# Kernel tuning notes

Measured on AMD Instinct MI355X. Metric: run time of the kernel, lower is better.

## Reference

```python
import jax, jax.numpy as jnp
import numpy as np

N, E, S, TS = 12, 7, 1024, 3          # num_boxes, edge_types, state_dim, time_step
D_IN = 1056 * 1 * 5 * 5               # emb_features * continuous_frames * crop_size^2


def _gru(x, h0, Wih, Whh, bih, bhh):
    """PyTorch-order GRU (gates r,z,n) over leading time axis. x: [T, B, S]."""
    def step(h, xt):
        gi = xt @ Wih.T + bih
        gh = h @ Whh.T + bhh
        ir, iz, inn = jnp.split(gi, 3, axis=-1)
        hr, hz, hn = jnp.split(gh, 3, axis=-1)
        r = jax.nn.sigmoid(ir + hr)
        z = jax.nn.sigmoid(iz + hz)
        n = jnp.tanh(inn + r * hn)
        h_new = (1.0 - z) * n + z * h
        return h_new, h_new
    _, ys = jax.lax.scan(step, h0, x)
    return ys


def _forward(pose_features, Wc, bc, We, be, Wcomp, bcomp, Wr, br, Wz, bz, Wh, bh,
             Wih, Whh, bih, bhh, Wa, ba):
    B, T = pose_features.shape[:2]
    BT, BNN = B * T, B * N * N
    # compress_fc: [BT, N, D_IN] -> [BT, N, S]
    prop = pose_features.reshape(BT, N, D_IN) @ Wc.T + bc
    # torch code xavier-normal-inits the GRU h0 each call; we use deterministic keys.
    h0_std = (2.0 / (BNN * S + S)) ** 0.5
    base = jax.random.key(42)
    gs = None
    for t in range(TS + 1):
        # all edge_fcs at once: [BT, N, E, S]
        msgs = jnp.einsum('bnd,esd->bnes', prop, We) + be
        msg_flat = msgs.reshape(BT, N * E, S)       # index n*E+e, matches torch cat+view
        scs = []
        for e in range(E):
            rf = msgs[:, :, e, :]                   # [BT, N, S]
            pair = jnp.concatenate([
                jnp.broadcast_to(rf[:, :, None, :], (BT, N, N, S)),
                jnp.broadcast_to(rf[:, None, :, :], (BT, N, N, S))], axis=-1)
            # -> [T, B*N*N, 2S] (permute(1,0,2,3,4) in torch)
            pair = pair.reshape(B, T, N, N, 2 * S).transpose(1, 0, 2, 3, 4).reshape(T, BNN, 2 * S)
            x = pair @ Wcomp.T + bcomp              # compress: [T, BNN, S]
            h0 = jax.random.normal(jax.random.fold_in(base, t * E + e), (BNN, S), dtype=x.dtype) * h0_std
            y = _gru(x, h0, Wih, Whh, bih, bhh)     # [T, BNN, S]
            y = y.reshape(T, B, N, N, S).transpose(1, 0, 2, 3, 4).reshape(BT, N, N, S)
            # edge attention (Dropout is identity in eval): sigmoid(linear->1)
            scs.append(jax.nn.sigmoid(jnp.einsum('bmns,s->bmn', y, Wa[e]) + ba[e]))
        gs = jnp.stack(scs, axis=-1)                # [BT, N, N, E]
        merged = jnp.einsum('bnm,bms->bns', gs.reshape(BT, N, N * E), msg_flat)
        a = jnp.concatenate([merged, prop], axis=-1)
        r = jax.nn.sigmoid(a @ Wr.T + br)
        z = jax.nn.sigmoid(a @ Wz.T + bz)
        h_hat = jnp.tanh(jnp.concatenate([merged, r * prop], axis=-1) @ Wh.T + bh)
        prop = (1.0 - z) * prop + z * h_hat
    box_states = gs                                 # last graph_scores
    action_score = ((1.0 - box_states[..., :1]) * box_states).sum(axis=2).reshape(B, T, N, E)
    actor_score = (1.0 - box_states[..., 0]).reshape(B, T, N, N)
    acty_score = jax.nn.softmax(
        (action_score * actor_score.sum(axis=-1)[..., None]).sum(axis=2)[:, :, 1:], axis=-1)
    return action_score, acty_score, actor_score


def setup_inputs() -> dict:
    key = jax.random.key(0)
    ks = jax.random.split(key, 16)
    B, T = 2, 4
    k = 1.0 / np.sqrt(S)  # torch GRU default uniform init bound
    return {
        'pose_features': jax.random.normal(ks[0], (B, T, N, D_IN), jnp.float32),
        'boxes_in': jax.random.uniform(ks[1], (B, T, N, 4), jnp.float32),
        'boxes_dhdw': jax.random.normal(ks[2], (B, T, N, 2), jnp.float32),
        'bboxes_num_in': jax.random.randint(ks[3], (B, T), 1, N),
        'actor_label': jax.random.randint(ks[4], (B, T, N), 0, E),
        'Wc': 0.01 * jax.random.normal(ks[5], (S, D_IN), jnp.float32),
        'bc': jnp.zeros((S,), jnp.float32),
        'We': 0.01 * jax.random.normal(ks[6], (E, S, S), jnp.float32),
        'be': jnp.zeros((E, S), jnp.float32),
        'Wcomp': 0.01 * jax.random.normal(ks[7], (S, 2 * S), jnp.float32),
        'bcomp': jnp.zeros((S,), jnp.float32),
        'Wr': 0.01 * jax.random.normal(ks[8], (S, 2 * S), jnp.float32),
        'br': jnp.zeros((S,), jnp.float32),
        'Wz': 0.01 * jax.random.normal(ks[9], (S, 2 * S), jnp.float32),
        'bz': jnp.zeros((S,), jnp.float32),
        'Wh': 0.01 * jax.random.normal(ks[10], (S, 2 * S), jnp.float32),
        'bh': jnp.zeros((S,), jnp.float32),
        'Wih': jax.random.uniform(ks[11], (3 * S, S), jnp.float32, -k, k),
        'Whh': jax.random.uniform(ks[12], (3 * S, S), jnp.float32, -k, k),
        'bih': jax.random.uniform(ks[13], (3 * S,), jnp.float32, -k, k),
        'bhh': jax.random.uniform(ks[14], (3 * S,), jnp.float32, -k, k),
        'Wa': 0.01 * jax.random.normal(ks[15], (E, S), jnp.float32),
        'ba': jnp.zeros((E,), jnp.float32),
    }


def reference(pose_features, boxes_in, boxes_dhdw, bboxes_num_in, actor_label,
              Wc, bc, We, be, Wcomp, bcomp, Wr, br, Wz, bz, Wh, bh,
              Wih, Whh, bih, bhh, Wa, ba):
    # boxes_in / boxes_dhdw / bboxes_num_in / actor_label only provide shapes in eval mode
    del boxes_in, boxes_dhdw, bboxes_num_in, actor_label
    return _forward(pose_features, Wc, bc, We, be, Wcomp, bcomp, Wr, br, Wz, bz,
                    Wh, bh, Wih, Whh, bih, bhh, Wa, ba)
```

## Files before the change

kernel.cpp:

```cpp
#include <hip/hip_runtime.h>
#include <math.h>

#define NQ 12
#define EQ 7
#define SQ 1024
#define TSQ 3
#define DIN 26400
#define BQ 2
#define TQ 4
#define BT 8
#define BNN 288
#define NROWS 2016
#define G3S 3072
#define BK 32

typedef unsigned short u16;
typedef float f32x4 __attribute__((ext_vector_type(4)));
typedef short s16x8 __attribute__((ext_vector_type(8)));

__device__ __forceinline__ short bh(float f) {
    unsigned u = __float_as_uint(f);
    return (short)((u + 0x8000u) >> 16);
}
__device__ __forceinline__ float b2f(u16 u) {
    return __uint_as_float((unsigned)u << 16);
}
__device__ __forceinline__ s16x8 pack8(float4 a, float4 b) {
    s16x8 r;
    r[0] = bh(a.x); r[1] = bh(a.y); r[2] = bh(a.z); r[3] = bh(a.w);
    r[4] = bh(b.x); r[5] = bh(b.y); r[6] = bh(b.z); r[7] = bh(b.w);
    return r;
}
__device__ __forceinline__ void gload16(const void* g, void* l) {
    __builtin_amdgcn_global_load_lds(
        (const __attribute__((address_space(1))) unsigned*)g,
        (__attribute__((address_space(3))) unsigned*)l, 16, 0, 0);
}
__device__ inline float sigmoidf(float x) { return 1.f / (1.f + expf(-x)); }

template<int AS32, int BS32>
__global__ __launch_bounds__(256)
void gemm_mfma(const void* __restrict__ Ap, long sAb, int lda,
               const void* __restrict__ Bp, long sBb, int ldb,
               const float* __restrict__ bias, long sBiasb,
               float* __restrict__ C, long sCb, int ldc,
               u16* __restrict__ Cb, long sCbb, int ldcb,
               int M, int Nn, int K, int act, int ksplit)
{
    __shared__ __align__(16) u16 lA[2][256][8];
    __shared__ __align__(16) u16 lB[2][512][8];

    const int z = blockIdx.z;
    const int az = z / ksplit;
    const int ks = z - az * ksplit;
    const int Ksl = K / ksplit;
    const int kbase = ks * Ksl;

    const char* Abase = (const char*)Ap + (long)az * sAb * (AS32 ? 4 : 2);
    const char* Bbase = (const char*)Bp + (long)az * sBb * (BS32 ? 4 : 2);

    const int tid = threadIdx.x;
    const int lane = tid & 63;
    const int wave = tid >> 6;
    const int row0 = blockIdx.x * 64;
    const int col0 = blockIdx.y * 128;
    const int wcol = wave * 32;

    const int akg = tid >> 6;
    long arow = row0 + (tid & 63); if (arow >= M) arow = M - 1;
    const int bkg0 = tid >> 7;
    const int s1 = tid + 256;
    const int bkg1 = s1 >> 7;
    long brow0 = col0 + (tid & 127); if (brow0 >= Nn) brow0 = Nn - 1;
    long brow1 = col0 + (s1 & 127);  if (brow1 >= Nn) brow1 = Nn - 1;

    const int arw32 = tid >> 2, akg32 = tid & 3;
    long ar32 = row0 + arw32; if (ar32 >= M) ar32 = M - 1;
    const int brw32 = tid >> 1, bh32 = tid & 1;
    long br32 = col0 + brw32; if (br32 >= Nn) br32 = Nn - 1;

    f32x4 acc[4][2] = {};

#define STAGE(b, kt) do {                                                     \
    const int k0_ = kbase + (kt) * BK;                                        \
    if constexpr (AS32) {                                                     \
        const float* A32 = (const float*)Abase;                               \
        const float* p0 = A32 + ar32 * lda + k0_ + akg32 * 8;                 \
        *(s16x8*)&lA[b][akg32 * 64 + arw32][0] =                              \
            pack8(*(const float4*)p0, *(const float4*)(p0 + 4));              \
    } else {                                                                  \
        const u16* A16 = (const u16*)Abase;                                   \
        gload16(A16 + arow * lda + k0_ + akg * 8, &lA[b][tid][0]);            \
    }                                                                         \
    if constexpr (BS32) {                                                     \
        const float* B32 = (const float*)Bbase;                               \
        const float* q0 = B32 + br32 * ldb + k0_ + bh32 * 16;                 \
        *(s16x8*)&lB[b][(bh32 * 2) * 128 + brw32][0] =                        \
            pack8(*(const float4*)q0, *(const float4*)(q0 + 4));              \
        *(s16x8*)&lB[b][(bh32 * 2 + 1) * 128 + brw32][0] =                    \
            pack8(*(const float4*)(q0 + 8), *(const float4*)(q0 + 12));       \
    } else {                                                                  \
        const u16* B16 = (const u16*)Bbase;                                   \
        gload16(B16 + brow0 * ldb + k0_ + bkg0 * 8, &lB[b][tid][0]);          \
        gload16(B16 + brow1 * ldb + k0_ + bkg1 * 8, &lB[b][s1][0]);           \
    }                                                                         \
} while (0)

    const int nk = Ksl / BK;
    STAGE(0, 0);
    __syncthreads();
    int buf = 0;
    const int kg = lane >> 4;
    const int lr = lane & 15;
    for (int kt = 0; kt < nk; ++kt) {
        if (kt + 1 < nk) STAGE(buf ^ 1, kt + 1);
        s16x8 af[4], bfr[2];
#pragma unroll
        for (int m = 0; m < 4; ++m)
            af[m] = *(const s16x8*)&lA[buf][kg * 64 + m * 16 + lr][0];
#pragma unroll
        for (int n = 0; n < 2; ++n)
            bfr[n] = *(const s16x8*)&lB[buf][kg * 128 + wcol + n * 16 + lr][0];
#pragma unroll
        for (int m = 0; m < 4; ++m)
#pragma unroll
            for (int n = 0; n < 2; ++n)
                acc[m][n] = __builtin_amdgcn_mfma_f32_16x16x32_bf16(af[m], bfr[n], acc[m][n], 0, 0, 0);
        __syncthreads();
        buf ^= 1;
    }
#undef STAGE

    const int ccol = lane & 15;
    const int crow = (lane >> 4) * 4;
#pragma unroll
    for (int n = 0; n < 2; ++n) {
        const int c = col0 + wcol + n * 16 + ccol;
        const float bv = bias ? bias[(long)az * sBiasb + c] : 0.f;
#pragma unroll
        for (int m = 0; m < 4; ++m) {
            const int rb = row0 + m * 16 + crow;
#pragma unroll
            for (int q = 0; q < 4; ++q) {
                const int r = rb + q;
                if (r >= M) continue;
                float v = acc[m][n][q] + bv;
                if (act == 1) v = 1.f / (1.f + expf(-v));
                else if (act == 2) v = tanhf(v);
                if (C)  C[(long)z * sCb + (long)r * ldc + c] = v;
                if (Cb) Cb[(long)z * sCbb + (long)r * ldcb + c] = (u16)bh(v);
            }
        }
    }
}

__global__ __launch_bounds__(256)
void gemm128_f32(const float* __restrict__ A, int lda,
                 const float* __restrict__ Bm, int ldb,
                 float* __restrict__ C, long sCb, int ldc,
                 u16* __restrict__ Cb, int ldcb,
                 int M, int Nn, int K, int ksplit)
{
    __shared__ __align__(16) u16 lA[2][512][8];
    __shared__ __align__(16) u16 lB[2][512][8];

    const int ks = blockIdx.z;
    const int Ksl = K / ksplit;
    const int kbase = ks * Ksl;

    const int tid = threadIdx.x;
    const int lane = tid & 63;
    const int wave = tid >> 6;
    const int row0 = blockIdx.x * 128;
    const int col0 = blockIdx.y * 128;
    const int wrow = (wave >> 1) * 64;
    const int wcol = (wave & 1) * 64;

    const int rw = tid >> 1, hf = tid & 1;
    long ar = row0 + rw; if (ar >= M) ar = M - 1;
    long br = col0 + rw; if (br >= Nn) br = Nn - 1;

    f32x4 acc[4][4] = {};

#define STAGE128(b, kt) do {                                                  \
    const int k0_ = kbase + (kt) * BK;                                        \
    const float* p = A + ar * lda + k0_ + hf * 16;                            \
    *(s16x8*)&lA[b][(hf * 2) * 128 + rw][0] =                                 \
        pack8(*(const float4*)p, *(const float4*)(p + 4));                    \
    *(s16x8*)&lA[b][(hf * 2 + 1) * 128 + rw][0] =                             \
        pack8(*(const float4*)(p + 8), *(const float4*)(p + 12));             \
    const float* q = Bm + br * ldb + k0_ + hf * 16;                           \
    *(s16x8*)&lB[b][(hf * 2) * 128 + rw][0] =                                 \
        pack8(*(const float4*)q, *(const float4*)(q + 4));                    \
    *(s16x8*)&lB[b][(hf * 2 + 1) * 128 + rw][0] =                             \
        pack8(*(const float4*)(q + 8), *(const float4*)(q + 12));             \
} while (0)

    const int nk = Ksl / BK;
    STAGE128(0, 0);
    __syncthreads();
    int buf = 0;
    const int kg = lane >> 4;
    const int lr = lane & 15;
    for (int kt = 0; kt < nk; ++kt) {
        if (kt + 1 < nk) STAGE128(buf ^ 1, kt + 1);
        s16x8 af[4], bfr[4];
#pragma unroll
        for (int m = 0; m < 4; ++m)
            af[m] = *(const s16x8*)&lA[buf][kg * 128 + wrow + m * 16 + lr][0];
#pragma unroll
        for (int n = 0; n < 4; ++n)
            bfr[n] = *(const s16x8*)&lB[buf][kg * 128 + wcol + n * 16 + lr][0];
#pragma unroll
        for (int m = 0; m < 4; ++m)
#pragma unroll
            for (int n = 0; n < 4; ++n)
                acc[m][n] = __builtin_amdgcn_mfma_f32_16x16x32_bf16(af[m], bfr[n], acc[m][n], 0, 0, 0);
        __syncthreads();
        buf ^= 1;
    }
#undef STAGE128

    const int ccol = lane & 15;
    const int crow = (lane >> 4) * 4;
#pragma unroll
    for (int n = 0; n < 4; ++n) {
        const int c = col0 + wcol + n * 16 + ccol;
#pragma unroll
        for (int m = 0; m < 4; ++m) {
            const int rb = row0 + wrow + m * 16 + crow;
#pragma unroll
            for (int q = 0; q < 4; ++q) {
                const int r = rb + q;
                if (r >= M) continue;
                float v = acc[m][n][q];
                if (C)  C[(long)ks * sCb + (long)r * ldc + c] = v;
                if (Cb) Cb[(long)r * ldcb + c] = (u16)bh(v);
            }
        }
    }
}

__global__ __launch_bounds__(512)
void gh_gru(const u16* __restrict__ hb_in, const u16* __restrict__ Whh_b,
            const float* __restrict__ bhh, const u16* __restrict__ Gnm_b,
            const float* __restrict__ cbias,
            float* __restrict__ h, u16* __restrict__ hb_out,
            const float* __restrict__ Wa, float* __restrict__ gs_part, int tt)
{
    __shared__ __align__(16) u16 lA[2][1024][8];
    __shared__ __align__(16) u16 lB[2][1536][8];
    __shared__ float rowdot[128];

    const int f = blockIdx.x;
    const int ly = 2 * (f & 7) + ((f >> 3) & 1);
    const int lx = f >> 4;
    const int row0 = lx * 128;
    const int col0 = ly * 64;

    const int tid = threadIdx.x;
    const int lane = tid & 63;
    const int wave = tid >> 6;
    const int wr = wave >> 1;
    const int wc = wave & 1;

    long arow = row0 + (tid & 127); if (arow >= NROWS) arow = NROWS - 1;

    const u16* aP0 = hb_in + arow * SQ + (tid >> 7) * 8;
    const u16* aP1 = aP0 + 32;
    const u16* bP[3];
#pragma unroll
    for (int j = 0; j < 3; ++j) {
        const int s = tid + j * 512;
        const int bk16 = s / 192;
        const int grow = s - bk16 * 192;
        bP[j] = Whh_b + (long)((grow >> 6) * SQ + col0 + (grow & 63)) * SQ + bk16 * 8;
    }

    f32x4 acc[3][2][2] = {};

#define GSTAGE(b, kt) do {                                                    \
    const int k0_ = (kt) * 64;                                                \
    gload16(aP0 + k0_, &lA[b][tid][0]);                                       \
    gload16(aP1 + k0_, &lA[b][tid + 512][0]);                                 \
    _Pragma("unroll")                                                         \
    for (int j = 0; j < 3; ++j)                                               \
        gload16(bP[j] + k0_, &lB[b][tid + j * 512][0]);                       \
} while (0)

    GSTAGE(0, 0);
    __syncthreads();
    int buf = 0;
    const int kg = lane >> 4;
    const int lr = lane & 15;
    for (int kt = 0; kt < 16; ++kt) {
        if (kt + 1 < 16) GSTAGE(buf ^ 1, kt + 1);
#pragma unroll
        for (int kk = 0; kk < 2; ++kk) {
            const int k16 = kk * 4 + kg;
            s16x8 af[2], bfr[3][2];
#pragma unroll
            for (int m = 0; m < 2; ++m)
                af[m] = *(const s16x8*)&lA[buf][k16 * 128 + wr * 32 + m * 16 + lr][0];
#pragma unroll
            for (int g = 0; g < 3; ++g)
#pragma unroll
                for (int n = 0; n < 2; ++n)
                    bfr[g][n] = *(const s16x8*)&lB[buf][k16 * 192 + g * 64 + wc * 32 + n * 16 + lr][0];
#pragma unroll
            for (int g = 0; g < 3; ++g)
#pragma unroll
                for (int m = 0; m < 2; ++m)
#pragma unroll
                    for (int n = 0; n < 2; ++n)
                        acc[g][m][n] = __builtin_amdgcn_mfma_f32_16x16x32_bf16(af[m], bfr[g][n], acc[g][m][n], 0, 0, 0);
        }
        __syncthreads();
        buf ^= 1;
    }
#undef GSTAGE

    if (tid < 128) rowdot[tid] = 0.f;
    __syncthreads();

    const int ccol = lane & 15;
    const int crow4 = (lane >> 4) * 4;
    int col2[2];
    float cbv[3][2], bhv[3][2];
#pragma unroll
    for (int n = 0; n < 2; ++n) {
        const int c = col0 + wc * 32 + n * 16 + ccol;
        col2[n] = c;
#pragma unroll
        for (int g = 0; g < 3; ++g) {
            cbv[g][n] = cbias[g * SQ + c];
            bhv[g][n] = bhh[g * SQ + c];
        }
    }

#pragma unroll
    for (int m = 0; m < 2; ++m) {
#pragma unroll
        for (int q = 0; q < 4; ++q) {
            const int row = row0 + wr * 32 + m * 16 + crow4 + q;
            const bool valid = (row < NROWS);
            float d = 0.f;
            if (valid) {
                const int e = row / BNN;
                const int rr = row - e * BNN;
                const int b_ = rr / 144;
                const int ni = (rr / 12) % 12;
                const int mi = rr % 12;
                const int bt = b_ * TQ + tt;
                const u16* gnp = Gnm_b + ((long)e * 96 + bt * 12 + ni) * 6144;
                const u16* gmp = Gnm_b + ((long)e * 96 + bt * 12 + mi) * 6144 + G3S;
                const float* wap = Wa + (long)e * SQ;
#pragma unroll
                for (int n = 0; n < 2; ++n) {
                    const int c = col2[n];
                    float gr  = acc[0][m][n][q] + bhv[0][n] + b2f(gnp[c]) + b2f(gmp[c]) + cbv[0][n];
                    float gz  = acc[1][m][n][q] + bhv[1][n] + b2f(gnp[SQ + c]) + b2f(gmp[SQ + c]) + cbv[1][n];
                    float ghn = acc[2][m][n][q] + bhv[2][n];
                    float gin = b2f(gnp[2 * SQ + c]) + b2f(gmp[2 * SQ + c]) + cbv[2][n];
                    float rg = sigmoidf(gr);
                    float zg = sigmoidf(gz);
                    float nn2 = tanhf(gin + rg * ghn);
                    float hp = h[(long)row * SQ + c];
                    float hn = (1.f - zg) * nn2 + zg * hp;
                    h[(long)row * SQ + c] = hn;
                    hb_out[(long)row * SQ + c] = (u16)bh(hn);
                    d += hn * wap[c];
                }
            }
            d += __shfl_xor(d, 1); d += __shfl_xor(d, 2);
            d += __shfl_xor(d, 4); d += __shfl_xor(d, 8);
            if (valid && ccol == 0)
                atomicAdd(&rowdot[wr * 32 + m * 16 + crow4 + q], d);
        }
    }
    __syncthreads();
    if (tid < 128) {
        const int row = row0 + tid;
        if (row < NROWS) gs_part[((long)tt * 2048 + row) * 16 + ly] = rowdot[tid];
    }
}

__global__ __launch_bounds__(256)
void gru0(const u16* __restrict__ Gnm_b, const float* __restrict__ cbias,
          const float* __restrict__ bhh,
          float* __restrict__ h, u16* __restrict__ hb_out,
          const float* __restrict__ Wa, const float* __restrict__ ba,
          float* __restrict__ gs)
{
    const int row = blockIdx.x;
    const int e = row / BNN;
    const int r = row % BNN;
    const int b_ = r / 144;
    const int ni = (r / 12) % 12;
    const int mi = r % 12;
    const int bt = b_ * TQ;

    const u16* gnp = Gnm_b + ((long)e * 96 + bt * 12 + ni) * 6144;
    const u16* gmp = Gnm_b + ((long)e * 96 + bt * 12 + mi) * 6144 + G3S;
    float* hp = h + (long)row * SQ;
    u16* hpb = hb_out + (long)row * SQ;

    const int s = threadIdx.x * 4;

    ushort4 nR = *(const ushort4*)(gnp + s);
    ushort4 nZ = *(const ushort4*)(gnp + SQ + s);
    ushort4 nN = *(const ushort4*)(gnp + 2 * SQ + s);
    ushort4 mR = *(const ushort4*)(gmp + s);
    ushort4 mZ = *(const ushort4*)(gmp + SQ + s);
    ushort4 mN = *(const ushort4*)(gmp + 2 * SQ + s);
    float4 cbR = *(const float4*)(cbias + s);
    float4 cbZ = *(const float4*)(cbias + SQ + s);
    float4 cbN = *(const float4*)(cbias + 2 * SQ + s);
    float4 bhR = *(const float4*)(bhh + s);
    float4 bhZ = *(const float4*)(bhh + SQ + s);
    float4 bhN = *(const float4*)(bhh + 2 * SQ + s);
    float4 wv  = *(const float4*)(Wa + (long)e * SQ + s);

    float4 hn4;
    float dot = 0.f;

#define GRU0_COMP(c, u)                                                       \
    {                                                                         \
        float rg = sigmoidf(b2f(nR.u) + b2f(mR.u) + cbR.c + bhR.c);           \
        float zg = sigmoidf(b2f(nZ.u) + b2f(mZ.u) + cbZ.c + bhZ.c);           \
        float nn = tanhf(b2f(nN.u) + b2f(mN.u) + cbN.c + rg * bhN.c);         \
        float hn = (1.f - zg) * nn;                                           \
        hn4.c = hn;                                                           \
        dot += hn * wv.c;                                                     \
    }
    GRU0_COMP(x, x) GRU0_COMP(y, y) GRU0_COMP(z, z) GRU0_COMP(w, w)
#undef GRU0_COMP

    *(float4*)(hp + s) = hn4;
    ushort4 hb4;
    hb4.x = (u16)bh(hn4.x); hb4.y = (u16)bh(hn4.y);
    hb4.z = (u16)bh(hn4.z); hb4.w = (u16)bh(hn4.w);
    *(ushort4*)(hpb + s) = hb4;

    for (int off = 32; off > 0; off >>= 1) dot += __shfl_down(dot, off);
    __shared__ float red[4];
    if ((threadIdx.x & 63) == 0) red[threadIdx.x >> 6] = dot;
    __syncthreads();
    if (threadIdx.x == 0) {
        float tot = red[0] + red[1] + red[2] + red[3] + ba[e];
        gs[((bt * 12 + ni) * 12 + mi) * EQ + e] = sigmoidf(tot);
    }
}

__global__ void gs_fin_all(const float* __restrict__ gs_part, const float* __restrict__ ba,
                           float* __restrict__ gs)
{
    int idx = blockIdx.x * 256 + threadIdx.x;
    if (idx >= 3 * 2048) return;
    const int tt = 1 + (idx >> 11);
    const int row = idx & 2047;
    if (row >= NROWS) return;
    float s = 0.f;
#pragma unroll
    for (int j = 0; j < 16; ++j) s += gs_part[((long)tt * 2048 + row) * 16 + j];
    const int e = row / BNN;
    const int rr = row - e * BNN;
    const int b_ = rr / 144;
    const int ni = (rr / 12) % 12;
    const int mi = rr % 12;
    const int bt = b_ * TQ + tt;
    gs[((bt * 12 + ni) * 12 + mi) * EQ + e] = sigmoidf(s + ba[e]);
}

__global__ __launch_bounds__(256)
void reduce_k(const float* __restrict__ part, int ksplit, int mn, int Nn,
              const float* __restrict__ bias, long sBiasB, int act,
              float* __restrict__ Cf, long sCfB, int ldcf,
              u16* __restrict__ Cb, long sCbB, int ldcb)
{
    int i4 = blockIdx.x * 256 + threadIdx.x;
    int total4 = mn >> 2;
    if (i4 >= total4) return;
    int b = blockIdx.y;
    const float4* p4 = (const float4*)part;
    float4 s = make_float4(0.f, 0.f, 0.f, 0.f);
    for (int ks = 0; ks < ksplit; ++ks) {
        float4 v = p4[(long)(b * ksplit + ks) * total4 + i4];
        s.x += v.x; s.y += v.y; s.z += v.z; s.w += v.w;
    }
    int i = i4 << 2;
    int r = i / Nn, c = i % Nn;
    if (bias) {
        float4 bv = *(const float4*)(bias + (long)b * sBiasB + c);
        s.x += bv.x; s.y += bv.y; s.z += bv.z; s.w += bv.w;
    }
    if (act == 1) {
        s.x = sigmoidf(s.x); s.y = sigmoidf(s.y); s.z = sigmoidf(s.z); s.w = sigmoidf(s.w);
    } else if (act == 2) {
        s.x = tanhf(s.x); s.y = tanhf(s.y); s.z = tanhf(s.z); s.w = tanhf(s.w);
    }
    if (Cf) *(float4*)(Cf + (long)b * sCfB + (long)r * ldcf + c) = s;
    if (Cb) {
        ushort4 o;
        o.x = (u16)bh(s.x); o.y = (u16)bh(s.y); o.z = (u16)bh(s.z); o.w = (u16)bh(s.w);
        *(ushort4*)(Cb + (long)b * sCbB + (long)r * ldcb + c) = o;
    }
}

__global__ void cvt_bf16_k(const float* __restrict__ src, u16* __restrict__ dst, int n4)
{
    int i = blockIdx.x * 256 + threadIdx.x;
    if (i >= n4) return;
    float4 v = ((const float4*)src)[i];
    ushort4 o;
    o.x = (u16)bh(v.x); o.y = (u16)bh(v.y); o.z = (u16)bh(v.z); o.w = (u16)bh(v.w);
    ((ushort4*)dst)[i] = o;
}

__global__ __launch_bounds__(256)
void transpose_wc(const float* __restrict__ Wcomp, float* __restrict__ W1T, float* __restrict__ W2T)
{
    __shared__ float t1[32][33];
    __shared__ float t2[32][33];
    const int tx = threadIdx.x & 31;
    const int ty = threadIdx.x >> 5;
    const int d0 = blockIdx.x * 32;
    const int s0 = blockIdx.y * 32;
#pragma unroll
    for (int k = 0; k < 4; ++k) {
        int d = d0 + ty + k * 8;
        t1[ty + k * 8][tx] = Wcomp[(long)d * 2048 + s0 + tx];
        t2[ty + k * 8][tx] = Wcomp[(long)d * 2048 + 1024 + s0 + tx];
    }
    __syncthreads();
#pragma unroll
    for (int k = 0; k < 4; ++k) {
        int s = s0 + ty + k * 8;
        W1T[(long)s * 1024 + d0 + tx] = t1[tx][ty + k * 8];
        W2T[(long)s * 1024 + d0 + tx] = t2[tx][ty + k * 8];
    }
}

__global__ void pack_rz(const float* __restrict__ Wr, const float* __restrict__ Wz,
                        const float* __restrict__ br, const float* __restrict__ bz,
                        u16* __restrict__ Wrz, float* __restrict__ brz)
{
    int i4 = blockIdx.x * 256 + threadIdx.x;
    if (i4 < 512) {
        int c = i4 * 4;
        float4 b = (c < 1024) ? *(const float4*)(br + c) : *(const float4*)(bz + c - 1024);
        *(float4*)(brz + c) = b;
    }
    if (i4 >= 1048576) return;
    int i = i4 * 4;
    int j = i >> 11;
    int c = i & 2047;
    float4 v = (j < 1024) ? *(const float4*)(Wr + (long)j * 2048 + c)
                          : *(const float4*)(Wz + (long)(j - 1024) * 2048 + c);
    ushort4 o;
    o.x = (u16)bh(v.x); o.y = (u16)bh(v.y); o.z = (u16)bh(v.z); o.w = (u16)bh(v.w);
    *(ushort4*)(Wrz + i) = o;
}

__global__ void cbias_k(const float* __restrict__ Wih, const float* __restrict__ bih,
                        const float* __restrict__ bcomp, float* __restrict__ cbias)
{
    int g = blockIdx.x * blockDim.x + threadIdx.x;
    if (g >= G3S) return;
    const float* w = Wih + (long)g * SQ;
    float s = 0.f;
    for (int k = 0; k < SQ; k += 4) {
        float4 wv = *(const float4*)(w + k);
        float4 bv = *(const float4*)(bcomp + k);
        s += wv.x * bv.x + wv.y * bv.y + wv.z * bv.z + wv.w * bv.w;
    }
    cbias[g] = s + bih[g];
}

__global__ __launch_bounds__(256)
void merged_amat_k(const float* __restrict__ gs, const u16* __restrict__ msgs_b,
                   const float* __restrict__ prop, u16* __restrict__ amat_b)
{
    const int bn = blockIdx.x;
    const int bt = bn / 12;
    __shared__ float g[84];
    if (threadIdx.x < 84) g[threadIdx.x] = gs[bn * 84 + threadIdx.x];
    __syncthreads();
    const int s = threadIdx.x * 4;
    float4 acc = make_float4(0.f, 0.f, 0.f, 0.f);
    for (int j = 0; j < 84; ++j) {
        const ushort4 mv = *(const ushort4*)(msgs_b + ((long)(bt * 84 + j)) * SQ + s);
        float gj = g[j];
        acc.x += gj * b2f(mv.x);
        acc.y += gj * b2f(mv.y);
        acc.z += gj * b2f(mv.z);
        acc.w += gj * b2f(mv.w);
    }
    ushort4 o;
    o.x = (u16)bh(acc.x); o.y = (u16)bh(acc.y); o.z = (u16)bh(acc.z); o.w = (u16)bh(acc.w);
    *(ushort4*)(amat_b + (long)bn * 2048 + s) = o;
    float4 pv = *(const float4*)(prop + (long)bn * SQ + s);
    ushort4 o2;
    o2.x = (u16)bh(pv.x); o2.y = (u16)bh(pv.y); o2.z = (u16)bh(pv.z); o2.w = (u16)bh(pv.w);
    *(ushort4*)(amat_b + (long)bn * 2048 + 1024 + s) = o2;
}

__global__ void ahat_k(const float* __restrict__ rz, const float* __restrict__ prop,
                       u16* __restrict__ amat_b)
{
    int i = blockIdx.x * 256 + threadIdx.x;
    int rrow = i >> 10, c = i & 1023;
    float r = rz[(long)rrow * 2048 + c];
    amat_b[(long)rrow * 2048 + 1024 + c] = (u16)bh(r * prop[i]);
}

__global__ void propupd_k(const float* __restrict__ rz, const float* __restrict__ hhat,
                          float* __restrict__ prop, u16* __restrict__ prop_b)
{
    int i = blockIdx.x * 256 + threadIdx.x;
    int rrow = i >> 10, c = i & 1023;
    float z = rz[(long)rrow * 2048 + 1024 + c];
    float v = (1.f - z) * prop[i] + z * hhat[i];
    prop[i] = v;
    prop_b[i] = (u16)bh(v);
}

__global__ __launch_bounds__(256)
void outputs_k(const float* __restrict__ gs, float* __restrict__ out)
{
    __shared__ float s_act[672];
    __shared__ float s_asum[96];
    int tid = threadIdx.x;
    for (int idx = tid; idx < 672; idx += 256) {
        int bn = idx / 7, e = idx % 7;
        float sum = 0.f;
        for (int m = 0; m < 12; ++m) {
            float g0 = gs[bn * 84 + m * 7];
            sum += (1.f - g0) * gs[bn * 84 + m * 7 + e];
        }
        s_act[idx] = sum;
        out[idx] = sum;
    }
    for (int idx = tid; idx < 96; idx += 256) {
        float a = 0.f;
        for (int m = 0; m < 12; ++m) a += 1.f - gs[idx * 84 + m * 7];
        s_asum[idx] = a;
    }
    for (int idx = tid; idx < 1152; idx += 256) {
        int bn = idx / 12, m = idx % 12;
        out[720 + idx] = 1.f - gs[bn * 84 + m * 7];
    }
    __syncthreads();
    if (tid < 8) {
        float tmp[6];
        float mx = -1e30f;
        for (int e = 1; e < 7; ++e) {
            float sum = 0.f;
            for (int n = 0; n < 12; ++n) {
                int bn = tid * 12 + n;
                sum += s_act[bn * 7 + e] * s_asum[bn];
            }
            tmp[e - 1] = sum;
            mx = fmaxf(mx, sum);
        }
        float den = 0.f;
        for (int e = 0; e < 6; ++e) { tmp[e] = expf(tmp[e] - mx); den += tmp[e]; }
        for (int e = 0; e < 6; ++e) out[672 + tid * 6 + e] = tmp[e] / den;
    }
}

template<int AS32, int BS32>
static void launch_gemm(const void* A, long sAb, int lda,
                        const void* B, long sBb, int ldb,
                        const float* bias, long sBiasb,
                        float* C, long sCb, int ldc,
                        u16* Cb, long sCbb, int ldcb,
                        int M, int Nn, int K, int act, int batch, int ksplit,
                        hipStream_t stream)
{
    dim3 grid((M + 63) / 64, (Nn + 127) / 128, batch * ksplit);
    gemm_mfma<AS32, BS32><<<grid, dim3(256), 0, stream>>>(
        A, sAb, lda, B, sBb, ldb, bias, sBiasb, C, sCb, ldc, Cb, sCbb, ldcb,
        M, Nn, K, act, ksplit);
}

extern "C" void kernel_launch(void* const* d_in, const int* in_sizes, int n_in,
                              void* d_out, int out_size, void* d_ws, size_t ws_size,
                              hipStream_t stream)
{
    const float* pose  = (const float*)d_in[0];
    const float* Wc    = (const float*)d_in[5];
    const float* bc    = (const float*)d_in[6];
    const float* We    = (const float*)d_in[7];
    const float* be    = (const float*)d_in[8];
    const float* Wcomp = (const float*)d_in[9];
    const float* bcomp = (const float*)d_in[10];
    const float* Wr    = (const float*)d_in[11];
    const float* br    = (const float*)d_in[12];
    const float* Wz    = (const float*)d_in[13];
    const float* bz    = (const float*)d_in[14];
    const float* Wh    = (const float*)d_in[15];
    const float* bh_   = (const float*)d_in[16];
    const float* Wih   = (const float*)d_in[17];
    const float* Whh   = (const float*)d_in[18];
    const float* bih   = (const float*)d_in[19];
    const float* bhh   = (const float*)d_in[20];
    const float* Wa    = (const float*)d_in[21];
    const float* ba    = (const float*)d_in[22];

    float* ws = (float*)d_ws;
    float* prop    = ws;
    float* cbias   = prop + 98304;
    float* h       = cbias + 3072;
    float* scratch = h + 2064384;
    float* gs      = scratch + 8257536;
    float* rz      = gs + 8064;
    float* hhat    = rz + 196608;
    float* brz     = hhat + 98304;
    float* gs_part = brz + 2048;
    float* fend    = gs_part + 131072;
    u16* Whh_b  = (u16*)fend;
    u16* Wnm_b  = Whh_b + 3145728;
    u16* Wrz_b  = Wnm_b + 6291456;
    u16* Gnm_b  = Wrz_b + 4194304;
    u16* msgs_b = Gnm_b + 4128768;
    u16* h_b0   = msgs_b + 688128;
    u16* h_b1   = h_b0 + 2064384;
    u16* prop_b = h_b1 + 2064384;
    u16* amat_b = prop_b + 98304;
    u16* pose_b = amat_b + 196608;
    u16* Wc_b   = pose_b + 2534400;

    float* W1T = scratch;
    float* W2T = scratch + 1048576;

    hipLaunchKernelGGL(cvt_bf16_k, dim3(3072), dim3(256), 0, stream, Whh, Whh_b, 786432);
    hipLaunchKernelGGL(cvt_bf16_k, dim3(2475), dim3(256), 0, stream, pose, pose_b, 633600);
    hipLaunchKernelGGL(cvt_bf16_k, dim3(26400), dim3(256), 0, stream, Wc, Wc_b, 6758400);
    hipLaunchKernelGGL(cbias_k, dim3(12), dim3(256), 0, stream, Wih, bih, bcomp, cbias);
    hipLaunchKernelGGL(transpose_wc, dim3(32, 32), dim3(256), 0, stream, Wcomp, W1T, W2T);
    hipLaunchKernelGGL(pack_rz, dim3(4096), dim3(256), 0, stream, Wr, Wz, br, bz, Wrz_b, brz);
    gemm128_f32<<<dim3(24, 8, 1), dim3(256), 0, stream>>>(
        Wih, SQ, W1T, SQ, nullptr, 0, SQ, Wnm_b, SQ, G3S, SQ, SQ, 1);
    gemm128_f32<<<dim3(24, 8, 1), dim3(256), 0, stream>>>(
        Wih, SQ, W2T, SQ, nullptr, 0, SQ, Wnm_b + (long)G3S * SQ, SQ, G3S, SQ, SQ, 1);
    launch_gemm<0, 0>(pose_b, 0, DIN, Wc_b, 0, DIN, nullptr, 0,
                      scratch, 98304, SQ, nullptr, 0, 0, 96, SQ, DIN, 0, 1, 55, stream);
    hipLaunchKernelGGL(reduce_k, dim3(96, 1), dim3(256), 0, stream,
                       scratch, 55, 98304, SQ, bc, 0L, 0,
                       prop, 0L, SQ, prop_b, 0L, SQ);

    for (int t = 0; t <= TSQ; ++t) {
        launch_gemm<0, 1>(prop_b, 0, SQ, We, (long)SQ * SQ, SQ, nullptr, 0,
                          scratch, 98304, SQ, nullptr, 0, 0, 96, SQ, SQ, 0, EQ, 4, stream);
        hipLaunchKernelGGL(reduce_k, dim3(96, EQ), dim3(256), 0, stream,
                           scratch, 4, 98304, SQ, be, (long)SQ, 0,
                           (float*)nullptr, 0L, 0, msgs_b, (long)SQ, EQ * SQ);
        launch_gemm<0, 0>(msgs_b, SQ, EQ * SQ, Wnm_b, 0, SQ, nullptr, 0,
                          nullptr, 0, 0, Gnm_b, 589824, 6 * SQ, 96, 6 * SQ, SQ, 0, EQ, 1, stream);
        hipLaunchKernelGGL(gru0, dim3(NROWS), dim3(256), 0, stream,
                           Gnm_b, cbias, bhh, h, h_b0, Wa, ba, gs);
        for (int tt = 1; tt < TQ; ++tt) {
            const u16* hin = (tt & 1) ? h_b0 : h_b1;
            u16* hout = (tt & 1) ? h_b1 : h_b0;
            hipLaunchKernelGGL(gh_gru, dim3(256), dim3(512), 0, stream,
                               hin, Whh_b, bhh, Gnm_b, cbias, h, hout, Wa, gs_part, tt);
        }
        hipLaunchKernelGGL(gs_fin_all, dim3(24), dim3(256), 0, stream, gs_part, ba, gs);
        if (t < TSQ) {
            hipLaunchKernelGGL(merged_amat_k, dim3(96), dim3(256), 0, stream,
                               gs, msgs_b, prop, amat_b);
            launch_gemm<0, 0>(amat_b, 0, 2 * SQ, Wrz_b, 0, 2 * SQ, nullptr, 0,
                              scratch, 196608, 2 * SQ, nullptr, 0, 0, 96, 2 * SQ, 2 * SQ, 0, 1, 8, stream);
            hipLaunchKernelGGL(reduce_k, dim3(192, 1), dim3(256), 0, stream,
                               scratch, 8, 196608, 2 * SQ, brz, 0L, 1,
                               rz, 0L, 2 * SQ, (u16*)nullptr, 0L, 0);
            hipLaunchKernelGGL(ahat_k, dim3(384), dim3(256), 0, stream, rz, prop, amat_b);
            launch_gemm<0, 1>(amat_b, 0, 2 * SQ, Wh, 0, 2 * SQ, nullptr, 0,
                              scratch, 98304, SQ, nullptr, 0, 0, 96, SQ, 2 * SQ, 0, 1, 8, stream);
            hipLaunchKernelGGL(reduce_k, dim3(96, 1), dim3(256), 0, stream,
                               scratch, 8, 98304, SQ, bh_, 0L, 2,
                               hhat, 0L, SQ, (u16*)nullptr, 0L, 0);
            hipLaunchKernelGGL(propupd_k, dim3(384), dim3(256), 0, stream, rz, hhat, prop, prop_b);
        }
    }

    hipLaunchKernelGGL(outputs_k, dim3(1), dim3(256), 0, stream, gs, (float*)d_out);
}
```

Measured before the change: 1.181 ms.

## Drop fp32 GRU hidden state and fuse split-K reductions into gate kernels

The GRU kernels stop keeping an fp32 copy of the hidden state and read the previous state from the bf16 buffer instead, which removes a large fp32 read and write per step. Separately, the split-K reductions for the r/z and hhat GEMMs are fused with the elementwise ahat and prop-update kernels, so two launches and the rz/hhat intermediate buffers go away. The cost is extra precision loss, because the recurrence now carries its state in bf16.

```diff
diff --git a/kernel.cpp b/kernel.cpp
--- a/kernel.cpp
+++ b/kernel.cpp
@@ -245,7 +245,7 @@
 void gh_gru(const u16* __restrict__ hb_in, const u16* __restrict__ Whh_b,
             const float* __restrict__ bhh, const u16* __restrict__ Gnm_b,
             const float* __restrict__ cbias,
-            float* __restrict__ h, u16* __restrict__ hb_out,
+            u16* __restrict__ hb_out,
             const float* __restrict__ Wa, float* __restrict__ gs_part, int tt)
 {
     __shared__ __align__(16) u16 lA[2][1024][8];
@@ -365,9 +365,8 @@
                     float rg = sigmoidf(gr);
                     float zg = sigmoidf(gz);
                     float nn2 = tanhf(gin + rg * ghn);
-                    float hp = h[(long)row * SQ + c];
+                    float hp = b2f(hb_in[(long)row * SQ + c]);
                     float hn = (1.f - zg) * nn2 + zg * hp;
-                    h[(long)row * SQ + c] = hn;
                     hb_out[(long)row * SQ + c] = (u16)bh(hn);
                     d += hn * wap[c];
                 }
@@ -388,7 +387,7 @@
 __global__ __launch_bounds__(256)
 void gru0(const u16* __restrict__ Gnm_b, const float* __restrict__ cbias,
           const float* __restrict__ bhh,
-          float* __restrict__ h, u16* __restrict__ hb_out,
+          u16* __restrict__ hb_out,
           const float* __restrict__ Wa, const float* __restrict__ ba,
           float* __restrict__ gs)
 {
@@ -402,7 +401,6 @@
 
     const u16* gnp = Gnm_b + ((long)e * 96 + bt * 12 + ni) * 6144;
     const u16* gmp = Gnm_b + ((long)e * 96 + bt * 12 + mi) * 6144 + G3S;
-    float* hp = h + (long)row * SQ;
     u16* hpb = hb_out + (long)row * SQ;
 
     const int s = threadIdx.x * 4;
@@ -436,7 +434,6 @@
     GRU0_COMP(x, x) GRU0_COMP(y, y) GRU0_COMP(z, z) GRU0_COMP(w, w)
 #undef GRU0_COMP
 
-    *(float4*)(hp + s) = hn4;
     ushort4 hb4;
     hb4.x = (u16)bh(hn4.x); hb4.y = (u16)bh(hn4.y);
     hb4.z = (u16)bh(hn4.z); hb4.w = (u16)bh(hn4.w);
@@ -507,6 +504,41 @@
     }
 }
 
+__global__ __launch_bounds__(256)
+void rz_ahat_k(const float* __restrict__ part, const float* __restrict__ brz,
+               const float* __restrict__ prop, u16* __restrict__ amat_b,
+               float* __restrict__ zbuf)
+{
+    int i = blockIdx.x * 256 + threadIdx.x;
+    int rrow = i >> 10, c = i & 1023;
+    float sr = 0.f, sz = 0.f;
+#pragma unroll
+    for (int ks = 0; ks < 8; ++ks) {
+        const float* p = part + (long)ks * 196608 + (long)rrow * 2048;
+        sr += p[c]; sz += p[1024 + c];
+    }
+    float r = sigmoidf(sr + brz[c]);
+    float z = sigmoidf(sz + brz[1024 + c]);
+    amat_b[(long)rrow * 2048 + 1024 + c] = (u16)bh(r * prop[i]);
+    zbuf[i] = z;
+}
+
+__global__ __launch_bounds__(256)
+void hhat_prop_k(const float* __restrict__ part, const float* __restrict__ bh_,
+                 const float* __restrict__ zbuf,
+                 float* __restrict__ prop, u16* __restrict__ prop_b)
+{
+    int i = blockIdx.x * 256 + threadIdx.x;
+    float s = 0.f;
+#pragma unroll
+    for (int ks = 0; ks < 8; ++ks) s += part[(long)ks * 98304 + i];
+    float hhat = tanhf(s + bh_[i & 1023]);
+    float z = zbuf[i];
+    float v = (1.f - z) * prop[i] + z * hhat;
+    prop[i] = v;
+    prop_b[i] = (u16)bh(v);
+}
+
 __global__ void cvt_bf16_k(const float* __restrict__ src, u16* __restrict__ dst, int n4)
 {
     int i = blockIdx.x * 256 + threadIdx.x;
@@ -603,26 +635,6 @@
     ushort4 o2;
     o2.x = (u16)bh(pv.x); o2.y = (u16)bh(pv.y); o2.z = (u16)bh(pv.z); o2.w = (u16)bh(pv.w);
     *(ushort4*)(amat_b + (long)bn * 2048 + 1024 + s) = o2;
-}
-
-__global__ void ahat_k(const float* __restrict__ rz, const float* __restrict__ prop,
-                       u16* __restrict__ amat_b)
-{
-    int i = blockIdx.x * 256 + threadIdx.x;
-    int rrow = i >> 10, c = i & 1023;
-    float r = rz[(long)rrow * 2048 + c];
-    amat_b[(long)rrow * 2048 + 1024 + c] = (u16)bh(r * prop[i]);
-}
-
-__global__ void propupd_k(const float* __restrict__ rz, const float* __restrict__ hhat,
-                          float* __restrict__ prop, u16* __restrict__ prop_b)
-{
-    int i = blockIdx.x * 256 + threadIdx.x;
-    int rrow = i >> 10, c = i & 1023;
-    float z = rz[(long)rrow * 2048 + 1024 + c];
-    float v = (1.f - z) * prop[i] + z * hhat[i];
-    prop[i] = v;
-    prop_b[i] = (u16)bh(v);
 }
 
 __global__ __launch_bounds__(256)
@@ -711,12 +723,10 @@
     float* ws = (float*)d_ws;
     float* prop    = ws;
     float* cbias   = prop + 98304;
-    float* h       = cbias + 3072;
-    float* scratch = h + 2064384;
+    float* scratch = cbias + 3072;
     float* gs      = scratch + 8257536;
-    float* rz      = gs + 8064;
-    float* hhat    = rz + 196608;
-    float* brz     = hhat + 98304;
+    float* zbuf    = gs + 8064;
+    float* brz     = zbuf + 98304;
     float* gs_part = brz + 2048;
     float* fend    = gs_part + 131072;
     u16* Whh_b  = (u16*)fend;
@@ -759,12 +769,12 @@
         launch_gemm<0, 0>(msgs_b, SQ, EQ * SQ, Wnm_b, 0, SQ, nullptr, 0,
                           nullptr, 0, 0, Gnm_b, 589824, 6 * SQ, 96, 6 * SQ, SQ, 0, EQ, 1, stream);
         hipLaunchKernelGGL(gru0, dim3(NROWS), dim3(256), 0, stream,
-                           Gnm_b, cbias, bhh, h, h_b0, Wa, ba, gs);
+                           Gnm_b, cbias, bhh, h_b0, Wa, ba, gs);
         for (int tt = 1; tt < TQ; ++tt) {
             const u16* hin = (tt & 1) ? h_b0 : h_b1;
             u16* hout = (tt & 1) ? h_b1 : h_b0;
             hipLaunchKernelGGL(gh_gru, dim3(256), dim3(512), 0, stream,
-                               hin, Whh_b, bhh, Gnm_b, cbias, h, hout, Wa, gs_part, tt);
+                               hin, Whh_b, bhh, Gnm_b, cbias, hout, Wa, gs_part, tt);
         }
         hipLaunchKernelGGL(gs_fin_all, dim3(24), dim3(256), 0, stream, gs_part, ba, gs);
         if (t < TSQ) {
@@ -772,16 +782,12 @@
                                gs, msgs_b, prop, amat_b);
             launch_gemm<0, 0>(amat_b, 0, 2 * SQ, Wrz_b, 0, 2 * SQ, nullptr, 0,
                               scratch, 196608, 2 * SQ, nullptr, 0, 0, 96, 2 * SQ, 2 * SQ, 0, 1, 8, stream);
-            hipLaunchKernelGGL(reduce_k, dim3(192, 1), dim3(256), 0, stream,
-                               scratch, 8, 196608, 2 * SQ, brz, 0L, 1,
-                               rz, 0L, 2 * SQ, (u16*)nullptr, 0L, 0);
-            hipLaunchKernelGGL(ahat_k, dim3(384), dim3(256), 0, stream, rz, prop, amat_b);
+            hipLaunchKernelGGL(rz_ahat_k, dim3(384), dim3(256), 0, stream,
+                               scratch, brz, prop, amat_b, zbuf);
             launch_gemm<0, 1>(amat_b, 0, 2 * SQ, Wh, 0, 2 * SQ, nullptr, 0,
                               scratch, 98304, SQ, nullptr, 0, 0, 96, SQ, 2 * SQ, 0, 1, 8, stream);
-            hipLaunchKernelGGL(reduce_k, dim3(96, 1), dim3(256), 0, stream,
-                               scratch, 8, 98304, SQ, bh_, 0L, 2,
-                               hhat, 0L, SQ, (u16*)nullptr, 0L, 0);
-            hipLaunchKernelGGL(propupd_k, dim3(384), dim3(256), 0, stream, rz, hhat, prop, prop_b);
+            hipLaunchKernelGGL(hhat_prop_k, dim3(384), dim3(256), 0, stream,
+                               scratch, bh_, zbuf, prop, prop_b);
         }
     }
 
```

Measured after the change: 1.135 ms. 3.9% less time.
